# Optimization experiments

Hardware: AMD Instinct MI355X
Metric: run time of the kernel (lower is better)

Reference implementation:

```python
import jax, jax.numpy as jnp
import numpy as np
import math

B, S, D, H = 4, 2048, 768, 12
DK = D // H

def setup_inputs() -> dict:
    key = jax.random.key(0)
    ks = jax.random.split(key, 12)
    sc = 1.0 / math.sqrt(D)
    return {
        'Q': jax.random.normal(ks[0], (B, S, D), jnp.float32),
        'K': jax.random.normal(ks[1], (B, S, D), jnp.float32),
        'V': jax.random.normal(ks[2], (B, S, D), jnp.float32),
        'mask': jax.random.randint(ks[3], (B, 1, S, S), 0, 2, jnp.int32),
        'Wq': jax.random.normal(ks[4], (D, D), jnp.float32) * sc,
        'bq': jnp.zeros((D,), jnp.float32),
        'Wk': jax.random.normal(ks[5], (D, D), jnp.float32) * sc,
        'bk': jnp.zeros((D,), jnp.float32),
        'Wv': jax.random.normal(ks[6], (D, D), jnp.float32) * sc,
        'bv': jnp.zeros((D,), jnp.float32),
        'Wo': jax.random.normal(ks[7], (D, D), jnp.float32) * sc,
        'bo': jnp.zeros((D,), jnp.float32),
    }

def _split_heads(x):
    # [B,S,D] -> [B,H,S,DK]
    return x.reshape(B, S, H, DK).transpose(0, 2, 1, 3)

def reference(Q, K, V, mask, Wq, bq, Wk, bk, Wv, bv, Wo, bo):
    q = _split_heads(Q @ Wq.T + bq)
    k = _split_heads(K @ Wk.T + bk)
    v = _split_heads(V @ Wv.T + bv)
    scores = jnp.einsum('bhqd,bhkd->bhqk', q, k) / math.sqrt(DK)
    # Faithful to the source: masked positions are filled with -1e-9 (NOT -inf)
    scores = jnp.where(mask == 0, jnp.float32(-1e-9), scores)
    attn = jax.nn.softmax(scores, axis=-1)
    x = jnp.einsum('bhqk,bhkd->bhqd', attn, v)          # [B,H,S,DK]
    x = x.transpose(0, 2, 1, 3).reshape(B, S, D)         # [B,S,D]
    return x @ Wo.T + bo
```

## Files before the change

### kernel.cpp

```cpp
#include <hip/hip_runtime.h>

#define BB 4
#define SS 2048
#define DD 768
#define HH 12
#define DKK 64
#define MM (BB*SS)

typedef __attribute__((ext_vector_type(8))) short bf16x8;
typedef __attribute__((ext_vector_type(4))) float f32x4;

#define GLDS(g, l) __builtin_amdgcn_global_load_lds( \
    (const __attribute__((address_space(1))) unsigned int*)(g), \
    (__attribute__((address_space(3))) unsigned int*)(l), 16, 0, 0)

__device__ __forceinline__ unsigned short f2bf(float f) {
    union { float f; unsigned int u; } v; v.f = f;
    unsigned int r = v.u + 0x7fffu + ((v.u >> 16) & 1u);
    return (unsigned short)(r >> 16);
}

#define NACT4 (MM*DD/4)
#define ABLK  (NACT4/256)
#define NW4   (DD*DD/4)
#define WBLK  (NW4/256)
#define MBLK  (BB*SS*SS/256)

__global__ void prep(
    const float* __restrict__ Q, const float* __restrict__ K, const float* __restrict__ V,
    const float* __restrict__ Wq, const float* __restrict__ Wk, const float* __restrict__ Wv,
    const float* __restrict__ Wo, const int* __restrict__ mask,
    unsigned short* __restrict__ Qc, unsigned short* __restrict__ Kc, unsigned short* __restrict__ Vc,
    unsigned short* __restrict__ Wqc, unsigned short* __restrict__ Wkc, unsigned short* __restrict__ Wvc,
    unsigned short* __restrict__ Woc, unsigned int* __restrict__ mbits)
{
    const int bx = blockIdx.x;
    if (bx < 3 * ABLK) {
        const int seg = bx / ABLK;
        const float* s = seg == 0 ? Q : seg == 1 ? K : V;
        unsigned short* d = seg == 0 ? Qc : seg == 1 ? Kc : Vc;
        const int i = (bx - seg * ABLK) * 256 + threadIdx.x;
        float4 v = ((const float4*)s)[i];
        ushort4 o;
        o.x = f2bf(v.x); o.y = f2bf(v.y); o.z = f2bf(v.z); o.w = f2bf(v.w);
        ((ushort4*)d)[i] = o;
    } else if (bx < 3 * ABLK + 4 * WBLK) {
        const int b2 = bx - 3 * ABLK;
        const int seg = b2 / WBLK;
        const float* s = seg == 0 ? Wq : seg == 1 ? Wk : seg == 2 ? Wv : Wo;
        unsigned short* d = seg == 0 ? Wqc : seg == 1 ? Wkc : seg == 2 ? Wvc : Woc;
        const int i = (b2 - seg * WBLK) * 256 + threadIdx.x;
        float4 v = ((const float4*)s)[i];
        ushort4 o;
        o.x = f2bf(v.x); o.y = f2bf(v.y); o.z = f2bf(v.z); o.w = f2bf(v.w);
        ((ushort4*)d)[i] = o;
    } else {
        const int t = (bx - (3 * ABLK + 4 * WBLK)) * 256 + threadIdx.x;
        const int m = mask[t];
        unsigned long long b = __ballot(m != 0);
        const int l = t & 63;
        if (l == 0)       mbits[t >> 5] = (unsigned int)b;
        else if (l == 32) mbits[t >> 5] = (unsigned int)(b >> 32);
    }
}

__global__ __launch_bounds__(256) void gemm_qkv(
    const unsigned short* __restrict__ Qc, const unsigned short* __restrict__ Kc, const unsigned short* __restrict__ Vc,
    const unsigned short* __restrict__ Wq, const unsigned short* __restrict__ Wk, const unsigned short* __restrict__ Wv,
    const float* __restrict__ bq, const float* __restrict__ bk, const float* __restrict__ bv,
    unsigned short* __restrict__ qb, unsigned short* __restrict__ kb, unsigned short* __restrict__ vt)
{
    __shared__ unsigned short As[128*32];
    __shared__ unsigned short Bs[128*32];
    const int mat = blockIdx.z;
    const unsigned short* X = mat == 0 ? Qc : mat == 1 ? Kc : Vc;
    const unsigned short* W = mat == 0 ? Wq : mat == 1 ? Wk : Wv;
    const float* bias        = mat == 0 ? bq : mat == 1 ? bk : bv;

    const int tid  = threadIdx.x;
    const int lane = tid & 63;
    const int w    = tid >> 6;
    const int wm   = w >> 1, wn = w & 1;
    const int quad = lane >> 4, c = lane & 15;
    const int m0 = blockIdx.y * 128, n0 = blockIdx.x * 128;

    f32x4 acc[4][4];
    #pragma unroll
    for (int i = 0; i < 4; i++)
        #pragma unroll
        for (int j = 0; j < 4; j++) acc[i][j] = (f32x4){0.f, 0.f, 0.f, 0.f};

    const int ch0 = tid, ch1 = 256 + tid;
    const int r0 = ch0 >> 2, cc0 = (ch0 & 3) << 3;
    const int r1 = ch1 >> 2, cc1 = (ch1 & 3) << 3;
    const unsigned short* Xg0 = X + (size_t)(m0 + r0) * DD + cc0;
    const unsigned short* Xg1 = X + (size_t)(m0 + r1) * DD + cc1;
    const unsigned short* Wg0 = W + (size_t)(n0 + r0) * DD + cc0;
    const unsigned short* Wg1 = W + (size_t)(n0 + r1) * DD + cc1;

    for (int k0 = 0; k0 < DD; k0 += 32) {
        GLDS(Xg0 + k0, As + ch0 * 8);
        GLDS(Xg1 + k0, As + ch1 * 8);
        GLDS(Wg0 + k0, Bs + ch0 * 8);
        GLDS(Wg1 + k0, Bs + ch1 * 8);
        __syncthreads();
        bf16x8 a[4], b[4];
        #pragma unroll
        for (int t = 0; t < 4; t++) {
            a[t] = *(const bf16x8*)(As + ((wm * 64 + t * 16 + c) * 32 + quad * 8));
            b[t] = *(const bf16x8*)(Bs + ((wn * 64 + t * 16 + c) * 32 + quad * 8));
        }
        #pragma unroll
        for (int tm = 0; tm < 4; tm++)
            #pragma unroll
            for (int tn = 0; tn < 4; tn++)
                acc[tm][tn] = __builtin_amdgcn_mfma_f32_16x16x32_bf16(a[tm], b[tn], acc[tm][tn], 0, 0, 0);
        __syncthreads();
    }

    if (mat < 2) {
        unsigned short* out = mat == 0 ? qb : kb;
        #pragma unroll
        for (int tn = 0; tn < 4; tn++) {
            const int col = n0 + wn * 64 + tn * 16 + c;
            const float bz = bias[col];
            #pragma unroll
            for (int tm = 0; tm < 4; tm++) {
                const int row = m0 + wm * 64 + tm * 16 + quad * 4;
                #pragma unroll
                for (int r = 0; r < 4; r++)
                    out[(size_t)(row + r) * DD + col] = f2bf(acc[tm][tn][r] + bz);
            }
        }
    } else {
        #pragma unroll
        for (int tn = 0; tn < 4; tn++) {
            const int col = n0 + wn * 64 + tn * 16 + c;
            const float bz = bias[col];
            const int h = col >> 6, dk = col & 63;
            #pragma unroll
            for (int tm = 0; tm < 4; tm++) {
                const int row = m0 + wm * 64 + tm * 16 + quad * 4;
                const int bb = row >> 11, s = row & 2047;
                ushort4 pk;
                pk.x = f2bf(acc[tm][tn][0] + bz);
                pk.y = f2bf(acc[tm][tn][1] + bz);
                pk.z = f2bf(acc[tm][tn][2] + bz);
                pk.w = f2bf(acc[tm][tn][3] + bz);
                *(ushort4*)(vt + ((((size_t)bb * HH + h) * DKK + dk) * SS + s)) = pk;
            }
        }
    }
}

#define EXPSCALE 0.18033688011112042f

__global__ __launch_bounds__(256, 3) void flash(
    const unsigned short* __restrict__ qb, const unsigned short* __restrict__ kb,
    const unsigned short* __restrict__ vt, const unsigned int* __restrict__ mbits,
    unsigned short* __restrict__ ob)
{
    __shared__ unsigned short Ks[2][2][64*32];
    __shared__ unsigned short Vs[2][2][64*32];
    __shared__ unsigned short Pb[4][32][72];

    const int bh = blockIdx.y;
    const int bi = bh / HH, h = bh % HH;
    const int tid  = threadIdx.x;
    const int w    = tid >> 6, lane = tid & 63;
    const int quad = lane >> 4, c = lane & 15;
    const int q0w = blockIdx.x * 128 + w * 32;

    bf16x8 qa[2][2];
    #pragma unroll
    for (int mt = 0; mt < 2; mt++) {
        const unsigned short* qbase = qb + (size_t)(bi * SS + q0w + mt * 16 + c) * DD + h * DKK + quad * 8;
        qa[mt][0] = *(const bf16x8*)(qbase);
        qa[mt][1] = *(const bf16x8*)(qbase + 32);
    }

    const int sr = tid >> 2, slot = tid & 3;
    const int lc = ((slot ^ (sr & 3)) << 3);
    const unsigned short* kgb = kb + ((size_t)bi * SS + sr) * DD + h * DKK + lc;
    const unsigned short* vgb = vt + (((size_t)bi * HH + h) * DKK + sr) * SS + lc;
    unsigned short* lds_k0[2] = { Ks[0][0] + tid * 8, Ks[1][0] + tid * 8 };
    unsigned short* lds_k1[2] = { Ks[0][1] + tid * 8, Ks[1][1] + tid * 8 };
    unsigned short* lds_v0[2] = { Vs[0][0] + tid * 8, Vs[1][0] + tid * 8 };
    unsigned short* lds_v1[2] = { Vs[0][1] + tid * 8, Vs[1][1] + tid * 8 };

    const unsigned int* mrow0 = mbits + (size_t)(bi * SS + q0w + c) * (SS / 32);
    const unsigned int* mrow1 = mrow0 + (size_t)16 * (SS / 32);

    f32x4 o[2][4];
    #pragma unroll
    for (int mt = 0; mt < 2; mt++)
        #pragma unroll
        for (int nt = 0; nt < 4; nt++) o[mt][nt] = (f32x4){0.f, 0.f, 0.f, 0.f};
    float rs[2] = {0.f, 0.f};

    const int sw = ((quad ^ (c & 3)) << 3);

    GLDS(kgb,      lds_k0[0]);
    GLDS(kgb + 32, lds_k1[0]);
    GLDS(vgb,      lds_v0[0]);
    GLDS(vgb + 32, lds_v1[0]);

    for (int t = 0; t < SS / 64; t++) {
        const int k0 = t * 64, par = t & 1;
        __syncthreads();
        if (t < SS / 64 - 1) {
            const unsigned short* kg = kgb + (size_t)(k0 + 64) * DD;
            const unsigned short* vg = vgb + (k0 + 64);
            GLDS(kg,      lds_k0[par ^ 1]);
            GLDS(kg + 32, lds_k1[par ^ 1]);
            GLDS(vg,      lds_v0[par ^ 1]);
            GLDS(vg + 32, lds_v1[par ^ 1]);
        }

        const uint2 mw0 = *(const uint2*)(mrow0 + (k0 >> 5));
        const uint2 mw1 = *(const uint2*)(mrow1 + (k0 >> 5));
        const unsigned long long mm[2] = {
            ((((unsigned long long)mw0.y << 32) | mw0.x) >> (quad * 4)),
            ((((unsigned long long)mw1.y << 32) | mw1.x) >> (quad * 4)) };

        #pragma unroll
        for (int nt = 0; nt < 4; nt++) {
            const bf16x8 kf0 = *(const bf16x8*)(&Ks[par][0][(nt * 16 + c) * 32 + sw]);
            const bf16x8 kf1 = *(const bf16x8*)(&Ks[par][1][(nt * 16 + c) * 32 + sw]);
            #pragma unroll
            for (int mt = 0; mt < 2; mt++) {
                f32x4 st = (f32x4){0.f, 0.f, 0.f, 0.f};
                st = __builtin_amdgcn_mfma_f32_16x16x32_bf16(kf0, qa[mt][0], st, 0, 0, 0);
                st = __builtin_amdgcn_mfma_f32_16x16x32_bf16(kf1, qa[mt][1], st, 0, 0, 0);
                const unsigned int mb = (unsigned int)(mm[mt] >> (nt * 16));
                unsigned int pk[2];
                #pragma unroll
                for (int r2 = 0; r2 < 2; r2++) {
                    float sv0 = st[r2 * 2]     * EXPSCALE;
                    float sv1 = st[r2 * 2 + 1] * EXPSCALE;
                    sv0 = (mb & (1u << (r2 * 2)))     ? sv0 : 0.0f;
                    sv1 = (mb & (1u << (r2 * 2 + 1))) ? sv1 : 0.0f;
                    const float p0 = __builtin_amdgcn_exp2f(sv0);
                    const float p1 = __builtin_amdgcn_exp2f(sv1);
                    rs[mt] += p0 + p1;
                    union { float f; unsigned int u; } u0, u1; u0.f = p0; u1.f = p1;
                    pk[r2] = __builtin_amdgcn_perm(u1.u + 0x8000u, u0.u + 0x8000u, 0x07060302);
                }
                *(uint2*)(&Pb[w][mt * 16 + c][nt * 16 + quad * 4]) = make_uint2(pk[0], pk[1]);
            }
        }

        bf16x8 pa[2][2];
        #pragma unroll
        for (int mt = 0; mt < 2; mt++) {
            pa[mt][0] = *(const bf16x8*)(&Pb[w][mt * 16 + c][quad * 8]);
            pa[mt][1] = *(const bf16x8*)(&Pb[w][mt * 16 + c][32 + quad * 8]);
        }
        #pragma unroll
        for (int nt = 0; nt < 4; nt++) {
            const bf16x8 vf0 = *(const bf16x8*)(&Vs[par][0][(nt * 16 + c) * 32 + sw]);
            const bf16x8 vf1 = *(const bf16x8*)(&Vs[par][1][(nt * 16 + c) * 32 + sw]);
            #pragma unroll
            for (int mt = 0; mt < 2; mt++) {
                o[mt][nt] = __builtin_amdgcn_mfma_f32_16x16x32_bf16(pa[mt][0], vf0, o[mt][nt], 0, 0, 0);
                o[mt][nt] = __builtin_amdgcn_mfma_f32_16x16x32_bf16(pa[mt][1], vf1, o[mt][nt], 0, 0, 0);
            }
        }
    }

    float rr[2][4];
    #pragma unroll
    for (int mt = 0; mt < 2; mt++) {
        float v = rs[mt];
        v += __shfl_xor(v, 16);
        v += __shfl_xor(v, 32);
        const float rn = __builtin_amdgcn_rcpf(v);
        #pragma unroll
        for (int reg = 0; reg < 4; reg++)
            rr[mt][reg] = __shfl(rn, quad * 4 + reg, 64);
    }

    #pragma unroll
    for (int mt = 0; mt < 2; mt++) {
        unsigned short* op = ob + (size_t)(bi * SS + q0w + mt * 16 + quad * 4) * DD + h * DKK + c;
        #pragma unroll
        for (int nt = 0; nt < 4; nt++)
            #pragma unroll
            for (int reg = 0; reg < 4; reg++)
                op[(size_t)reg * DD + nt * 16] = f2bf(o[mt][nt][reg] * rr[mt][reg]);
    }
}

__global__ __launch_bounds__(256) void gemm_out(
    const unsigned short* __restrict__ A, const unsigned short* __restrict__ W,
    const float* __restrict__ bias, float* __restrict__ out)
{
    __shared__ unsigned short As[128*32];
    __shared__ unsigned short Bs[128*32];
    const int tid  = threadIdx.x;
    const int lane = tid & 63;
    const int w    = tid >> 6;
    const int wm   = w >> 1, wn = w & 1;
    const int quad = lane >> 4, c = lane & 15;
    const int m0 = blockIdx.y * 128, n0 = blockIdx.x * 128;

    f32x4 acc[4][4];
    #pragma unroll
    for (int i = 0; i < 4; i++)
        #pragma unroll
        for (int j = 0; j < 4; j++) acc[i][j] = (f32x4){0.f, 0.f, 0.f, 0.f};

    const int ch0 = tid, ch1 = 256 + tid;
    const int r0 = ch0 >> 2, cc0 = (ch0 & 3) << 3;
    const int r1 = ch1 >> 2, cc1 = (ch1 & 3) << 3;
    const unsigned short* Ag0 = A + (size_t)(m0 + r0) * DD + cc0;
    const unsigned short* Ag1 = A + (size_t)(m0 + r1) * DD + cc1;
    const unsigned short* Wg0 = W + (size_t)(n0 + r0) * DD + cc0;
    const unsigned short* Wg1 = W + (size_t)(n0 + r1) * DD + cc1;

    for (int k0 = 0; k0 < DD; k0 += 32) {
        GLDS(Ag0 + k0, As + ch0 * 8);
        GLDS(Ag1 + k0, As + ch1 * 8);
        GLDS(Wg0 + k0, Bs + ch0 * 8);
        GLDS(Wg1 + k0, Bs + ch1 * 8);
        __syncthreads();
        bf16x8 a[4], b[4];
        #pragma unroll
        for (int t = 0; t < 4; t++) {
            a[t] = *(const bf16x8*)(As + ((wm * 64 + t * 16 + c) * 32 + quad * 8));
            b[t] = *(const bf16x8*)(Bs + ((wn * 64 + t * 16 + c) * 32 + quad * 8));
        }
        #pragma unroll
        for (int tm = 0; tm < 4; tm++)
            #pragma unroll
            for (int tn = 0; tn < 4; tn++)
                acc[tm][tn] = __builtin_amdgcn_mfma_f32_16x16x32_bf16(a[tm], b[tn], acc[tm][tn], 0, 0, 0);
        __syncthreads();
    }

    #pragma unroll
    for (int tn = 0; tn < 4; tn++) {
        const int col = n0 + wn * 64 + tn * 16 + c;
        const float bz = bias[col];
        #pragma unroll
        for (int tm = 0; tm < 4; tm++) {
            const int row = m0 + wm * 64 + tm * 16 + quad * 4;
            #pragma unroll
            for (int r = 0; r < 4; r++)
                out[(size_t)(row + r) * DD + col] = acc[tm][tn][r] + bz;
        }
    }
}

extern "C" void kernel_launch(void* const* d_in, const int* in_sizes, int n_in,
                              void* d_out, int out_size, void* d_ws, size_t ws_size,
                              hipStream_t stream) {
    (void)in_sizes; (void)n_in; (void)out_size; (void)ws_size;
    const float* Q    = (const float*)d_in[0];
    const float* K    = (const float*)d_in[1];
    const float* V    = (const float*)d_in[2];
    const int*   mask = (const int*)d_in[3];
    const float* Wq   = (const float*)d_in[4];
    const float* bq   = (const float*)d_in[5];
    const float* Wk   = (const float*)d_in[6];
    const float* bk   = (const float*)d_in[7];
    const float* Wv   = (const float*)d_in[8];
    const float* bv   = (const float*)d_in[9];
    const float* Wo   = (const float*)d_in[10];
    const float* bo   = (const float*)d_in[11];
    float* out = (float*)d_out;

    char* ws = (char*)d_ws;
    size_t off = 0;
    auto alloc = [&](size_t bytes) { char* p = ws + off; off += (bytes + 255) & ~255ULL; return p; };
    const size_t act = (size_t)MM * DD * 2;
    unsigned short* Qc  = (unsigned short*)alloc(act);
    unsigned short* Kc  = (unsigned short*)alloc(act);
    unsigned short* Vc  = (unsigned short*)alloc(act);
    unsigned short* Wqc = (unsigned short*)alloc((size_t)DD * DD * 2);
    unsigned short* Wkc = (unsigned short*)alloc((size_t)DD * DD * 2);
    unsigned short* Wvc = (unsigned short*)alloc((size_t)DD * DD * 2);
    unsigned short* Woc = (unsigned short*)alloc((size_t)DD * DD * 2);
    unsigned short* qb  = (unsigned short*)alloc(act);
    unsigned short* kb  = (unsigned short*)alloc(act);
    unsigned short* vt  = (unsigned short*)alloc(act);
    unsigned int*  mbits = (unsigned int*)alloc((size_t)BB * SS * (SS / 32) * 4);
    unsigned short* ob = Qc;

    prep<<<dim3(3 * ABLK + 4 * WBLK + MBLK), 256, 0, stream>>>(
        Q, K, V, Wq, Wk, Wv, Wo, mask, Qc, Kc, Vc, Wqc, Wkc, Wvc, Woc, mbits);
    gemm_qkv<<<dim3(DD / 128, MM / 128, 3), 256, 0, stream>>>(
        Qc, Kc, Vc, Wqc, Wkc, Wvc, bq, bk, bv, qb, kb, vt);
    flash<<<dim3(SS / 128, BB * HH), 256, 0, stream>>>(qb, kb, vt, mbits, ob);
    gemm_out<<<dim3(DD / 128, MM / 128), 256, 0, stream>>>(ob, Woc, bo, out);
}
```

Baseline: 374.0 us.

## Keep softmax P in registers by permuting K rows to match MFMA operand layout

The K tile is loaded into shared memory with its rows permuted so that the S=K·Q^T accumulator fragments line up directly with the B-operand layout of the P·V MFMA. This removes the per-warp Pb shared-memory round trip (store, then reload) for the probability tile. The PV product is transposed to V^T·P, which lets the output be written as row-contiguous ushort4 stores and drops the shuffles for the row normalizer. It also switches to single 64x64 K/V tiles with an 8-way XOR swizzle. The risk is correctness of the row permutation and mask-bit indexing, plus possible changes in register pressure.

New measurement: 376.4 us. About the same (+0.6%).

```diff
diff --git a/kernel.cpp b/kernel.cpp
--- a/kernel.cpp
+++ b/kernel.cpp
@@ -160,9 +160,8 @@
     const unsigned short* __restrict__ vt, const unsigned int* __restrict__ mbits,
     unsigned short* __restrict__ ob)
 {
-    __shared__ unsigned short Ks[2][2][64*32];
-    __shared__ unsigned short Vs[2][2][64*32];
-    __shared__ unsigned short Pb[4][32][72];
+    __shared__ unsigned short Ks[2][64*64];
+    __shared__ unsigned short Vs[2][64*64];
 
     const int bh = blockIdx.y;
     const int bi = bh / HH, h = bh % HH;
@@ -179,14 +178,15 @@
         qa[mt][1] = *(const bf16x8*)(qbase + 32);
     }
 
-    const int sr = tid >> 2, slot = tid & 3;
-    const int lc = ((slot ^ (sr & 3)) << 3);
-    const unsigned short* kgb = kb + ((size_t)bi * SS + sr) * DD + h * DKK + lc;
-    const unsigned short* vgb = vt + (((size_t)bi * HH + h) * DKK + sr) * SS + lc;
-    unsigned short* lds_k0[2] = { Ks[0][0] + tid * 8, Ks[1][0] + tid * 8 };
-    unsigned short* lds_k1[2] = { Ks[0][1] + tid * 8, Ks[1][1] + tid * 8 };
-    unsigned short* lds_v0[2] = { Vs[0][0] + tid * 8, Vs[1][0] + tid * 8 };
-    unsigned short* lds_v1[2] = { Vs[0][1] + tid * 8, Vs[1][1] + tid * 8 };
+    const int l0 = tid >> 3, sl = tid & 7;
+    const int l1 = 32 + l0;
+    const int lc = (sl ^ (l0 & 7)) << 3;
+    const int kp0 = ((l0 >> 5) << 5) | (((l0 >> 2) & 3) << 3) | (((l0 >> 4) & 1) << 2) | (l0 & 3);
+    const int kp1 = ((l1 >> 5) << 5) | (((l1 >> 2) & 3) << 3) | (((l1 >> 4) & 1) << 2) | (l1 & 3);
+    const unsigned short* kg0 = kb + ((size_t)bi * SS + kp0) * DD + h * DKK + lc;
+    const unsigned short* kg1 = kb + ((size_t)bi * SS + kp1) * DD + h * DKK + lc;
+    const unsigned short* vg0 = vt + (((size_t)bi * HH + h) * DKK + l0) * SS + lc;
+    const unsigned short* vg1 = vt + (((size_t)bi * HH + h) * DKK + l1) * SS + lc;
 
     const unsigned int* mrow0 = mbits + (size_t)(bi * SS + q0w + c) * (SS / 32);
     const unsigned int* mrow1 = mrow0 + (size_t)16 * (SS / 32);
@@ -195,99 +195,91 @@
     #pragma unroll
     for (int mt = 0; mt < 2; mt++)
         #pragma unroll
-        for (int nt = 0; nt < 4; nt++) o[mt][nt] = (f32x4){0.f, 0.f, 0.f, 0.f};
+        for (int dt = 0; dt < 4; dt++) o[mt][dt] = (f32x4){0.f, 0.f, 0.f, 0.f};
     float rs[2] = {0.f, 0.f};
 
-    const int sw = ((quad ^ (c & 3)) << 3);
-
-    GLDS(kgb,      lds_k0[0]);
-    GLDS(kgb + 32, lds_k1[0]);
-    GLDS(vgb,      lds_v0[0]);
-    GLDS(vgb + 32, lds_v1[0]);
+    const int cswz = c & 7;
+
+    GLDS(kg0, Ks[0] + (size_t)tid * 8);
+    GLDS(kg1, Ks[0] + (size_t)(256 + tid) * 8);
+    GLDS(vg0, Vs[0] + (size_t)tid * 8);
+    GLDS(vg1, Vs[0] + (size_t)(256 + tid) * 8);
 
     for (int t = 0; t < SS / 64; t++) {
         const int k0 = t * 64, par = t & 1;
         __syncthreads();
         if (t < SS / 64 - 1) {
-            const unsigned short* kg = kgb + (size_t)(k0 + 64) * DD;
-            const unsigned short* vg = vgb + (k0 + 64);
-            GLDS(kg,      lds_k0[par ^ 1]);
-            GLDS(kg + 32, lds_k1[par ^ 1]);
-            GLDS(vg,      lds_v0[par ^ 1]);
-            GLDS(vg + 32, lds_v1[par ^ 1]);
+            const size_t ko = (size_t)(k0 + 64);
+            GLDS(kg0 + ko * DD, Ks[par ^ 1] + (size_t)tid * 8);
+            GLDS(kg1 + ko * DD, Ks[par ^ 1] + (size_t)(256 + tid) * 8);
+            GLDS(vg0 + ko,      Vs[par ^ 1] + (size_t)tid * 8);
+            GLDS(vg1 + ko,      Vs[par ^ 1] + (size_t)(256 + tid) * 8);
         }
 
         const uint2 mw0 = *(const uint2*)(mrow0 + (k0 >> 5));
         const uint2 mw1 = *(const uint2*)(mrow1 + (k0 >> 5));
-        const unsigned long long mm[2] = {
-            ((((unsigned long long)mw0.y << 32) | mw0.x) >> (quad * 4)),
-            ((((unsigned long long)mw1.y << 32) | mw1.x) >> (quad * 4)) };
-
-        #pragma unroll
-        for (int nt = 0; nt < 4; nt++) {
-            const bf16x8 kf0 = *(const bf16x8*)(&Ks[par][0][(nt * 16 + c) * 32 + sw]);
-            const bf16x8 kf1 = *(const bf16x8*)(&Ks[par][1][(nt * 16 + c) * 32 + sw]);
-            #pragma unroll
-            for (int mt = 0; mt < 2; mt++) {
-                f32x4 st = (f32x4){0.f, 0.f, 0.f, 0.f};
-                st = __builtin_amdgcn_mfma_f32_16x16x32_bf16(kf0, qa[mt][0], st, 0, 0, 0);
-                st = __builtin_amdgcn_mfma_f32_16x16x32_bf16(kf1, qa[mt][1], st, 0, 0, 0);
-                const unsigned int mb = (unsigned int)(mm[mt] >> (nt * 16));
-                unsigned int pk[2];
+        const unsigned long long mmq[2] = {
+            ((((unsigned long long)mw0.y << 32) | mw0.x) >> (quad * 8)),
+            ((((unsigned long long)mw1.y << 32) | mw1.x) >> (quad * 8)) };
+
+        #pragma unroll
+        for (int p = 0; p < 2; p++) {
+            unsigned int pq[2][4];
+            #pragma unroll
+            for (int tt = 0; tt < 2; tt++) {
+                const unsigned short* kbase = &Ks[par][((2 * p + tt) * 16 + c) << 6];
+                const bf16x8 kf0 = *(const bf16x8*)(kbase + ((quad ^ cswz) << 3));
+                const bf16x8 kf1 = *(const bf16x8*)(kbase + (((4 + quad) ^ cswz) << 3));
                 #pragma unroll
-                for (int r2 = 0; r2 < 2; r2++) {
-                    float sv0 = st[r2 * 2]     * EXPSCALE;
-                    float sv1 = st[r2 * 2 + 1] * EXPSCALE;
-                    sv0 = (mb & (1u << (r2 * 2)))     ? sv0 : 0.0f;
-                    sv1 = (mb & (1u << (r2 * 2 + 1))) ? sv1 : 0.0f;
-                    const float p0 = __builtin_amdgcn_exp2f(sv0);
-                    const float p1 = __builtin_amdgcn_exp2f(sv1);
-                    rs[mt] += p0 + p1;
-                    union { float f; unsigned int u; } u0, u1; u0.f = p0; u1.f = p1;
-                    pk[r2] = __builtin_amdgcn_perm(u1.u + 0x8000u, u0.u + 0x8000u, 0x07060302);
+                for (int mt = 0; mt < 2; mt++) {
+                    f32x4 st = (f32x4){0.f, 0.f, 0.f, 0.f};
+                    st = __builtin_amdgcn_mfma_f32_16x16x32_bf16(kf0, qa[mt][0], st, 0, 0, 0);
+                    st = __builtin_amdgcn_mfma_f32_16x16x32_bf16(kf1, qa[mt][1], st, 0, 0, 0);
+                    const unsigned int mb = (unsigned int)(mmq[mt] >> (p * 32 + tt * 4)) & 15u;
+                    #pragma unroll
+                    for (int r2 = 0; r2 < 2; r2++) {
+                        float sv0 = st[r2 * 2]     * EXPSCALE;
+                        float sv1 = st[r2 * 2 + 1] * EXPSCALE;
+                        sv0 = (mb & (1u << (r2 * 2)))     ? sv0 : 0.0f;
+                        sv1 = (mb & (1u << (r2 * 2 + 1))) ? sv1 : 0.0f;
+                        const float p0 = __builtin_amdgcn_exp2f(sv0);
+                        const float p1 = __builtin_amdgcn_exp2f(sv1);
+                        rs[mt] += p0 + p1;
+                        union { float f; unsigned int u; } u0, u1; u0.f = p0; u1.f = p1;
+                        pq[mt][tt * 2 + r2] = __builtin_amdgcn_perm(u1.u + 0x8000u, u0.u + 0x8000u, 0x07060302);
+                    }
                 }
-                *(uint2*)(&Pb[w][mt * 16 + c][nt * 16 + quad * 4]) = make_uint2(pk[0], pk[1]);
             }
-        }
-
-        bf16x8 pa[2][2];
-        #pragma unroll
-        for (int mt = 0; mt < 2; mt++) {
-            pa[mt][0] = *(const bf16x8*)(&Pb[w][mt * 16 + c][quad * 8]);
-            pa[mt][1] = *(const bf16x8*)(&Pb[w][mt * 16 + c][32 + quad * 8]);
-        }
-        #pragma unroll
-        for (int nt = 0; nt < 4; nt++) {
-            const bf16x8 vf0 = *(const bf16x8*)(&Vs[par][0][(nt * 16 + c) * 32 + sw]);
-            const bf16x8 vf1 = *(const bf16x8*)(&Vs[par][1][(nt * 16 + c) * 32 + sw]);
-            #pragma unroll
-            for (int mt = 0; mt < 2; mt++) {
-                o[mt][nt] = __builtin_amdgcn_mfma_f32_16x16x32_bf16(pa[mt][0], vf0, o[mt][nt], 0, 0, 0);
-                o[mt][nt] = __builtin_amdgcn_mfma_f32_16x16x32_bf16(pa[mt][1], vf1, o[mt][nt], 0, 0, 0);
+            #pragma unroll
+            for (int dt = 0; dt < 4; dt++) {
+                const bf16x8 vf = *(const bf16x8*)(&Vs[par][((dt * 16 + c) << 6) + ((((p << 2) + quad) ^ cswz) << 3)]);
+                #pragma unroll
+                for (int mt = 0; mt < 2; mt++) {
+                    union { unsigned int u[4]; bf16x8 v; } pb;
+                    pb.u[0] = pq[mt][0]; pb.u[1] = pq[mt][1];
+                    pb.u[2] = pq[mt][2]; pb.u[3] = pq[mt][3];
+                    o[mt][dt] = __builtin_amdgcn_mfma_f32_16x16x32_bf16(vf, pb.v, o[mt][dt], 0, 0, 0);
+                }
             }
         }
     }
 
-    float rr[2][4];
     #pragma unroll
     for (int mt = 0; mt < 2; mt++) {
         float v = rs[mt];
         v += __shfl_xor(v, 16);
         v += __shfl_xor(v, 32);
         const float rn = __builtin_amdgcn_rcpf(v);
-        #pragma unroll
-        for (int reg = 0; reg < 4; reg++)
-            rr[mt][reg] = __shfl(rn, quad * 4 + reg, 64);
-    }
-
-    #pragma unroll
-    for (int mt = 0; mt < 2; mt++) {
-        unsigned short* op = ob + (size_t)(bi * SS + q0w + mt * 16 + quad * 4) * DD + h * DKK + c;
-        #pragma unroll
-        for (int nt = 0; nt < 4; nt++)
-            #pragma unroll
-            for (int reg = 0; reg < 4; reg++)
-                op[(size_t)reg * DD + nt * 16] = f2bf(o[mt][nt][reg] * rr[mt][reg]);
+        unsigned short* op = ob + (size_t)(bi * SS + q0w + mt * 16 + c) * DD + h * DKK + quad * 4;
+        #pragma unroll
+        for (int dt = 0; dt < 4; dt++) {
+            ushort4 pk;
+            pk.x = f2bf(o[mt][dt][0] * rn);
+            pk.y = f2bf(o[mt][dt][1] * rn);
+            pk.z = f2bf(o[mt][dt][2] * rn);
+            pk.w = f2bf(o[mt][dt][3] * rn);
+            *(ushort4*)(op + dt * 16) = pk;
+        }
     }
 }
 
```
